# Performance work log

Measured on AMD Instinct MI355X. Metric: run time of the kernel, lower is better.

Reference implementation:

```python
import jax, jax.numpy as jnp
import numpy as np

N, D, H1, K = 4096, 128, 256, 128


def setup_inputs() -> dict:
    key = jax.random.key(0)
    ks = jax.random.split(key, 8)
    A = jax.random.uniform(ks[3], (D, D), dtype=jnp.float32)
    A = A * (1.0 - jnp.eye(D, dtype=jnp.float32))  # DAG prob mask, no self-loops
    return {
        "x": jax.random.normal(ks[0], (N, D), dtype=jnp.float32),
        "weight": jax.random.normal(ks[1], (D, D), dtype=jnp.float32) * 0.1,
        "bias": jax.random.normal(ks[2], (1, D), dtype=jnp.float32) * 0.1,
        "A": A,
        "W1": jax.random.normal(ks[4], (D, H1), dtype=jnp.float32) * 0.1,
        "b1": jax.random.normal(ks[5], (H1,), dtype=jnp.float32) * 0.1,
        "W2": jax.random.normal(ks[6], (H1, K), dtype=jnp.float32) * 0.1,
        "b2": jax.random.normal(ks[7], (K,), dtype=jnp.float32) * 0.1,
    }


def reference(x, weight, bias, A, W1, b1, W2, b2):
    # to_adj (eval path): masked weights
    W = weight * A                                   # [D, D]
    y = x @ W + bias                                 # [N, D]
    # __expand__ builds diag(y[n]) [N,D,D]; since e[n,i,:] = y[n,i]*I[i,:],
    # the first Linear collapses to a per-row scaling of W1 (same math, fused):
    # e @ W1 -> y[n,i] * W1[i,:]
    h1 = jax.nn.relu(y[:, :, None] * W1[None, :, :] + b1)   # [N, D, H1]
    f = (h1 @ W2 + b2).sum(axis=2)                   # [N, D] (sum over output dim)
    # h_func, method='gnn'
    I = jnp.eye(D, dtype=x.dtype)
    A2 = jnp.square(W)
    M = I + A2 / D
    E = jnp.linalg.matrix_power(M, D - 1)
    h_val = (E.T * M).sum() - D
    # l1_reg (same prob mask in eval)
    reg = jnp.abs(W).sum()
    return (f, h_val, reg)
```

## Files before the change

kernel.cpp:

```cpp
#include <hip/hip_runtime.h>

#define NN 4096
#define DD 128
#define HH1 256

#define WS_S    0
#define WS_S2   16384
#define WS_S3   32768
#define WS_S4   49152
#define WS_W    65536
#define WS_B2S  82688
#define WS_TACC 82696
#define WS_DONE 82708
#define WS_REGP 82712
#define WS_XT   99328
#define WS_TH   623616
#define WS_A    656384
#define WS_B    689280
#define WS_YT   722176
#define WS_REQ_FLOATS 1246464
#define WS_REQ_BYTES  (WS_REQ_FLOATS * 4UL)

#define O_S    0
#define O_S2   16384
#define O_S3   32768
#define O_S4   49152
#define O_W2S  65536
#define O_B2S  65792
#define O_TACC 65808
#define O_DONE 65824
#define O_REGP 65840

__device__ __forceinline__ float waveReduce(float v) {
#pragma unroll
  for (int off = 32; off > 0; off >>= 1) v += __shfl_down(v, off, 64);
  return v;
}


__global__ __launch_bounds__(256) void kA4(
    const float* __restrict__ weight, const float* __restrict__ Amat,
    const float* __restrict__ b2, const float* __restrict__ x,
    float* __restrict__ ws) {
  const int b = blockIdx.x, tid = threadIdx.x;
  __shared__ float s_lds[DD * DD];
  if (b < 64) {
    const float4* w4 = (const float4*)weight;
    const float4* a4 = (const float4*)Amat;
    float4* s4 = (float4*)s_lds;
    const float inv = 1.0f / 128.0f;
    for (int e = tid; e < DD * DD / 4; e += 256) {
      float4 wv = w4[e], av = a4[e], o;
      float t;
      t = wv.x * av.x; o.x = t * t * inv;
      t = wv.y * av.y; o.y = t * t * inv;
      t = wv.z * av.z; o.z = t * t * inv;
      t = wv.w * av.w; o.w = t * t * inv;
      s4[e] = o;
    }
    __syncthreads();
    const int i = (b << 1) + (tid >> 7), j = tid & 127;
    const float* row = &s_lds[i * DD];
    float acc = 0.f;
#pragma unroll 8
    for (int k = 0; k < DD; ++k) acc = fmaf(row[k], s_lds[k * DD + j], acc);
    ws[WS_S2 + i * DD + j] = acc;
  } else if (b < 72) {
    const int base = (b - 64) * 2048;
    const float inv = 1.0f / 128.0f;
    for (int e = tid; e < 2048; e += 256) {
      const int idx = base + e;
      const float w = weight[idx] * Amat[idx];
      ws[WS_W + idx] = w;
      ws[WS_S + idx] = w * w * inv;
    }
  } else if (b == 72) {
    __shared__ float red[4];
    float v = (tid < 128) ? b2[tid] : 0.f;
    v = waveReduce(v);
    if ((tid & 63) == 0) red[tid >> 6] = v;
    __syncthreads();
    if (tid == 0) ws[WS_B2S] = (red[0] + red[1]) + (red[2] + red[3]);
    if (tid >= 64 && tid < 74) ws[WS_TACC + (tid - 64)] = 0.f;
    if (tid == 96) *(unsigned int*)(ws + WS_DONE) = 0u;
  } else if (b < 81) {
    const int bb = b - 73;
    const int base = bb * 2048;
    float s = 0.f;
    for (int e = tid; e < 2048; e += 256) {
      const int idx = base + e;
      s += fabsf(weight[idx] * Amat[idx]);
    }
    s = waveReduce(s);
    __shared__ float red2[4];
    if ((tid & 63) == 0) red2[tid >> 6] = s;
    __syncthreads();
    if (tid == 0) ws[WS_REGP + bb] = (red2[0] + red2[1]) + (red2[2] + red2[3]);
  } else {
    float* xs = s_lds;
    const int n0 = (b - 81) * 64;
    const float4* x4 = (const float4*)x;
    for (int e = tid; e < 2048; e += 256) {
      const int r = e >> 5, c = e & 31;
      const float4 v = x4[(n0 + r) * 32 + c];
      float* p = &xs[r * 133 + (c << 2)];
      p[0] = v.x; p[1] = v.y; p[2] = v.z; p[3] = v.w;
    }
    __syncthreads();
    float* xT = ws + WS_XT;
    const int c = tid & 15, ks = tid >> 4;
#pragma unroll
    for (int m = 0; m < 8; ++m) {
      const int k = ks + (m << 4);
      float4 o;
      o.x = xs[((c << 2) + 0) * 133 + k];
      o.y = xs[((c << 2) + 1) * 133 + k];
      o.z = xs[((c << 2) + 2) * 133 + k];
      o.w = xs[((c << 2) + 3) * 133 + k];
      *(float4*)&xT[k * NN + n0 + (c << 2)] = o;
    }
  }
}

__global__ __launch_bounds__(256) void kB5(const float* __restrict__ bias,
                                           const float* __restrict__ W1,
                                           const float* __restrict__ b1v,
                                           const float* __restrict__ W2,
                                           float* __restrict__ ws) {
  const int tid = threadIdx.x;
  if (blockIdx.x < 128) {
    const int sb = blockIdx.x;
    const bool isS4 = sb >= 64;
    const int mb = isS4 ? sb - 64 : sb;
    const float* __restrict__ L = ws + WS_S2;
    const float* __restrict__ R = ws + (isS4 ? WS_S2 : WS_S);
    float* __restrict__ O = ws + (isS4 ? WS_S4 : WS_S3);
    const int i = (mb << 1) + (tid >> 7), j = tid & 127;
    float acc = 0.f;
#pragma unroll 8
    for (int k = 0; k < DD; ++k) acc = fmaf(L[i * DD + k], R[k * DD + j], acc);
    O[i * DD + j] = acc;
    return;
  }
  if (blockIdx.x < 384) {
    const int kb = blockIdx.x - 128;
    const int n0 = (kb & 15) << 8, i0 = (kb >> 4) << 3;
    const int n = n0 + tid;
    const float* __restrict__ xT = ws + WS_XT;
    const float* __restrict__ Wm = ws + WS_W;
    float* __restrict__ yT = ws + WS_YT;
    float acc[8];
#pragma unroll
    for (int q = 0; q < 8; ++q) acc[q] = 0.f;
#pragma unroll 8
    for (int k = 0; k < DD; ++k) {
      const float xv = xT[k * NN + n];
      const float* Wk = Wm + k * DD + i0;
#pragma unroll
      for (int q = 0; q < 8; ++q) acc[q] = fmaf(Wk[q], xv, acc[q]);
    }
#pragma unroll
    for (int q = 0; q < 8; ++q) yT[(i0 + q) * NN + n] = acc[q] + bias[i0 + q];
    return;
  }
  const int i = blockIdx.x - 384;
  __shared__ float kT[256], kS[256], kC[256];
  __shared__ float redb[8];
  const int j = tid;
  const float4* r = (const float4*)(W2 + j * 128);
  float4 s4v = make_float4(0.f, 0.f, 0.f, 0.f);
#pragma unroll 8
  for (int k = 0; k < 32; ++k) {
    const float4 v = r[k];
    s4v.x += v.x; s4v.y += v.y; s4v.z += v.z; s4v.w += v.w;
  }
  const float w2s = (s4v.x + s4v.y) + (s4v.z + s4v.w);
  const float w = W1[i * HH1 + j];
  const float bj = b1v[j];
  const float s = w * w2s, c = bj * w2s;
  float th, ds, dc, bs, bc;
  if (w > 0.f) {
    th = -bj / w; ds = s; dc = c; bs = 0.f; bc = 0.f;
  } else if (w < 0.f) {
    th = -bj / w; ds = -s; dc = -c; bs = s; bc = c;
  } else {
    th = 3.4e38f; ds = 0.f; dc = 0.f; bs = 0.f; bc = fmaxf(bj, 0.f) * w2s;
  }
  {
    const float rs = waveReduce(bs), rc = waveReduce(bc);
    if ((tid & 63) == 0) {
      redb[tid >> 6] = rs;
      redb[4 + (tid >> 6)] = rc;
    }
  }
  kT[tid] = th; kS[tid] = ds; kC[tid] = dc;
  __syncthreads();
  const float b_s = (redb[0] + redb[1]) + (redb[2] + redb[3]);
  const float b_c = (redb[4] + redb[5]) + (redb[6] + redb[7]);
  int rank = 0;
  float accS = 0.f, accC = 0.f;
  for (int jj = 0; jj < 256; ++jj) {
    const float thj = kT[jj];
    const float dsj = kS[jj], dcj = kC[jj];
    const bool le = (thj < th) || (thj == th && jj <= j);
    if (le) {
      ++rank;
      accS += dsj;
      accC += dcj;
    }
  }
  ws[WS_TH + i * 256 + (rank - 1)] = th;
  ws[WS_A + i * 257 + rank] = b_s + accS;
  ws[WS_B + i * 257 + rank] = b_c + accC;
  if (tid == 0) {
    ws[WS_A + i * 257] = b_s;
    ws[WS_B + i * 257] = b_c;
  }
}

__global__ __launch_bounds__(256) void kC7(float* __restrict__ ws,
                                           float* __restrict__ out) {
  const int tid = threadIdx.x;
  if (blockIdx.x < 512) {
    __shared__ float lT[4 * 256];
    __shared__ float lA[4 * 257];
    __shared__ float lB[4 * 257];
    __shared__ float ts[256 * 5];
    const int fb = blockIdx.x;
    const int n0 = (fb >> 5) << 8, i0 = (fb & 31) << 2;
    const int w = tid >> 6, l = tid & 63;
    const int iu = __builtin_amdgcn_readfirstlane(i0 + w);

#pragma unroll
    for (int q = 0; q < 4; ++q) {
      lT[(q << 8) + tid] = ws[WS_TH + (i0 + q) * 256 + tid];
      lA[q * 257 + tid] = ws[WS_A + (i0 + q) * 257 + tid];
      lB[q * 257 + tid] = ws[WS_B + (i0 + q) * 257 + tid];
      if (tid == 0) {
        lA[q * 257 + 256] = ws[WS_A + (i0 + q) * 257 + 256];
        lB[q * 257 + 256] = ws[WS_B + (i0 + q) * 257 + 256];
      }
    }
    const float* __restrict__ yT = ws + WS_YT;
    const float4 yv = *(const float4*)&yT[iu * NN + n0 + (l << 2)];
    const float sb2 = ws[WS_B2S];
    __syncthreads();

    const float* Tw = &lT[w << 8];
    const float* Aw = &lA[w * 257];
    const float* Bw = &lB[w * 257];
    const float yq4[4] = {yv.x, yv.y, yv.z, yv.w};
#pragma unroll
    for (int q = 0; q < 4; ++q) {
      const float yq = yq4[q];
      int m = 0;
#pragma unroll
      for (int st = 128; st > 0; st >>= 1) {
        if (Tw[m + st - 1] <= yq) m += st;
      }
      const float f = fmaf(Aw[m], yq, Bw[m]) + sb2;
      ts[((l << 2) + q) * 5 + w] = f;
    }
    __syncthreads();
    const int m = tid;
    float4 o;
    o.x = ts[m * 5 + 0]; o.y = ts[m * 5 + 1];
    o.z = ts[m * 5 + 2]; o.w = ts[m * 5 + 3];
    *(float4*)&out[(n0 + m) * DD + i0] = o;
    return;
  }
  const int tb = blockIdx.x - 512;
  const int i = (tb << 1) + (tid >> 7), j = tid & 127;
  const float* S1 = ws + WS_S;
  const float* S2 = ws + WS_S2;
  const float* S3 = ws + WS_S3;
  const float* S4 = ws + WS_S4;
  const float a1 = S1[i * DD + j], a2 = S2[i * DD + j], a3 = S3[i * DD + j];
  const float b1t = S1[j * DD + i], b2t = S2[j * DD + i],
              b3t = S3[j * DD + i], b4t = S4[j * DD + i];
  float e7 = 0.f;
#pragma unroll 8
  for (int k = 0; k < DD; ++k) e7 = fmaf(S3[i * DD + k], S4[k * DD + j], e7);
  float c[10];
  c[0] = a1 * b1t; c[1] = a2 * b1t; c[2] = a2 * b2t; c[3] = a3 * b2t;
  c[4] = a3 * b3t; c[5] = a3 * b4t; c[6] = e7 * b1t; c[7] = e7 * b2t;
  c[8] = e7 * b3t; c[9] = e7 * b4t;
  __shared__ float red[4][10];
#pragma unroll
  for (int m = 0; m < 10; ++m) {
    const float v = waveReduce(c[m]);
    if ((tid & 63) == 0) red[tid >> 6][m] = v;
  }
  __syncthreads();
  if (tid == 0) {
    float* tacc = ws + WS_TACC;
    for (int m = 0; m < 10; ++m)
      atomicAdd(&tacc[m], (red[0][m] + red[1][m]) + (red[2][m] + red[3][m]));
    __threadfence();
    unsigned int* done = (unsigned int*)(ws + WS_DONE);
    const unsigned int old = atomicAdd(done, 1u);
    if (old == 63u) {
      __threadfence();
      double h = 0.0, C = 8128.0;
      for (int kk = 2; kk <= 11; ++kk) {
        const float tv = atomicAdd(&tacc[kk - 2], 0.0f);
        h += C * (double)tv;
        C = C * (double)(128 - kk) / (double)(kk + 1);
      }
      float reg = 0.f;
      for (int m = 0; m < 8; ++m) reg += ws[WS_REGP + m];
      out[NN * DD] = (float)h;
      out[NN * DD + 1] = reg;
    }
  }
}

__global__ __launch_bounds__(256) void kA_old(
    const float* __restrict__ weight, const float* __restrict__ Amat,
    const float* __restrict__ W2, const float* __restrict__ b2,
    float* __restrict__ ws) {
  const int b = blockIdx.x, tid = threadIdx.x;
  if (b < 64) {
    __shared__ float s_lds[DD * DD];
    const float4* w4 = (const float4*)weight;
    const float4* a4 = (const float4*)Amat;
    float4* s4 = (float4*)s_lds;
    const float inv = 1.0f / 128.0f;
    for (int e = tid; e < DD * DD / 4; e += 256) {
      float4 wv = w4[e], av = a4[e], o;
      float t;
      t = wv.x * av.x; o.x = t * t * inv;
      t = wv.y * av.y; o.y = t * t * inv;
      t = wv.z * av.z; o.z = t * t * inv;
      t = wv.w * av.w; o.w = t * t * inv;
      s4[e] = o;
    }
    __syncthreads();
    const int i = (b << 1) + (tid >> 7), j = tid & 127;
    const float* row = &s_lds[i * DD];
    float acc = 0.f;
#pragma unroll 8
    for (int k = 0; k < DD; ++k) acc = fmaf(row[k], s_lds[k * DD + j], acc);
    ws[O_S2 + i * DD + j] = acc;
  } else if (b < 72) {
    const int base = (b - 64) * 2048;
    const float inv = 1.0f / 128.0f;
    for (int e = tid; e < 2048; e += 256) {
      const int idx = base + e;
      const float w = weight[idx] * Amat[idx];
      ws[O_S + idx] = w * w * inv;
    }
  } else if (b == 72) {
    const float4* r = (const float4*)(W2 + tid * 128);
    float4 s4 = make_float4(0.f, 0.f, 0.f, 0.f);
#pragma unroll 8
    for (int k = 0; k < 32; ++k) {
      const float4 v = r[k];
      s4.x += v.x; s4.y += v.y; s4.z += v.z; s4.w += v.w;
    }
    ws[O_W2S + tid] = (s4.x + s4.y) + (s4.z + s4.w);
  } else if (b == 73) {
    __shared__ float red[4];
    float v = (tid < 128) ? b2[tid] : 0.f;
    v = waveReduce(v);
    if ((tid & 63) == 0) red[tid >> 6] = v;
    __syncthreads();
    if (tid == 0) ws[O_B2S] = (red[0] + red[1]) + (red[2] + red[3]);
    if (tid >= 64 && tid < 74) ws[O_TACC + (tid - 64)] = 0.f;
    if (tid == 96) *(unsigned int*)(ws + O_DONE) = 0u;
  } else {
    const int bb = b - 74;
    const int base = bb * 2048;
    float s = 0.f;
    for (int e = tid; e < 2048; e += 256) {
      const int idx = base + e;
      s += fabsf(weight[idx] * Amat[idx]);
    }
    s = waveReduce(s);
    __shared__ float red[4];
    if ((tid & 63) == 0) red[tid >> 6] = s;
    __syncthreads();
    if (tid == 0) ws[O_REGP + bb] = (red[0] + red[1]) + (red[2] + red[3]);
  }
}

__global__ __launch_bounds__(256) void kB_old(
    const float* __restrict__ x, const float* __restrict__ weight,
    const float* __restrict__ Amat, const float* __restrict__ bias,
    const float* __restrict__ W1, const float* __restrict__ b1v,
    float* __restrict__ ws, float* __restrict__ out) {
  const int tid = threadIdx.x;
  if (blockIdx.x < 128) {
    const int sb = blockIdx.x;
    const bool isS4 = sb >= 64;
    const int mb = isS4 ? sb - 64 : sb;
    const float* __restrict__ L = ws + O_S2;
    const float* __restrict__ R = ws + (isS4 ? O_S2 : O_S);
    float* __restrict__ O = ws + (isS4 ? O_S4 : O_S3);
    const int i = (mb << 1) + (tid >> 7), j = tid & 127;
    float acc = 0.f;
#pragma unroll 8
    for (int k = 0; k < DD; ++k) acc = fmaf(L[i * DD + k], R[k * DD + j], acc);
    O[i * DD + j] = acc;
    return;
  }
  __shared__ float xs[64 * 132];
  __shared__ float4 fq[4 * 256];
  __shared__ float wcol[4 * 128];
  __shared__ float ts[64 * 5];
  const int fb = blockIdx.x - 128;
  const int i0 = (fb & 31) << 2, n0 = (fb >> 5) << 6;
  const float4* x4 = (const float4*)x;
  for (int e = tid; e < 64 * 32; e += 256) {
    const int r = e >> 5, c = e & 31;
    *(float4*)&xs[r * 132 + (c << 2)] = x4[(n0 + r) * 32 + c];
  }
  for (int e = tid; e < 512; e += 256) {
    const int w = e >> 7, k = e & 127;
    const int gi = k * DD + i0 + w;
    wcol[(w << 7) + k] = weight[gi] * Amat[gi];
  }
  const float* w2s = ws + O_W2S;
  for (int e = tid; e < 1024; e += 256) {
    const int w = e >> 8, j = e & 255;
    fq[(w << 8) + j] = make_float4(W1[(i0 + w) * HH1 + j], b1v[j], w2s[j], 0.f);
  }
  __syncthreads();
  const int w = tid >> 6, l = tid & 63;
  float t = bias[i0 + w];
  const float4* xr = (const float4*)&xs[l * 132];
  const float4* wc = (const float4*)&wcol[w << 7];
#pragma unroll
  for (int k = 0; k < 32; ++k) {
    const float4 xv = xr[k], wv = wc[k];
    t = fmaf(xv.x, wv.x, t);
    t = fmaf(xv.y, wv.y, t);
    t = fmaf(xv.z, wv.z, t);
    t = fmaf(xv.w, wv.w, t);
  }
  float acc = ws[O_B2S];
  const float4* fp = &fq[w << 8];
#pragma unroll 8
  for (int j = 0; j < HH1; ++j) {
    const float4 c = fp[j];
    acc = fmaf(fmaxf(fmaf(t, c.x, c.y), 0.f), c.z, acc);
  }
  ts[l * 5 + w] = acc;
  __syncthreads();
  if (tid < 64) {
    const float4 o = make_float4(ts[tid * 5 + 0], ts[tid * 5 + 1],
                                 ts[tid * 5 + 2], ts[tid * 5 + 3]);
    *(float4*)&out[(n0 + tid) * DD + i0] = o;
  }
}

__global__ __launch_bounds__(256) void kC_old(float* __restrict__ ws,
                                              float* __restrict__ out) {
  const int tid = threadIdx.x;
  const int i = (blockIdx.x << 1) + (tid >> 7), j = tid & 127;
  const float* S1 = ws + O_S;
  const float* S2 = ws + O_S2;
  const float* S3 = ws + O_S3;
  const float* S4 = ws + O_S4;
  const float a1 = S1[i * DD + j], a2 = S2[i * DD + j], a3 = S3[i * DD + j];
  const float b1t = S1[j * DD + i], b2t = S2[j * DD + i],
              b3t = S3[j * DD + i], b4t = S4[j * DD + i];
  float e7 = 0.f;
#pragma unroll 8
  for (int k = 0; k < DD; ++k) e7 = fmaf(S3[i * DD + k], S4[k * DD + j], e7);
  float c[10];
  c[0] = a1 * b1t; c[1] = a2 * b1t; c[2] = a2 * b2t; c[3] = a3 * b2t;
  c[4] = a3 * b3t; c[5] = a3 * b4t; c[6] = e7 * b1t; c[7] = e7 * b2t;
  c[8] = e7 * b3t; c[9] = e7 * b4t;
  __shared__ float red[4][10];
#pragma unroll
  for (int m = 0; m < 10; ++m) {
    const float v = waveReduce(c[m]);
    if ((tid & 63) == 0) red[tid >> 6][m] = v;
  }
  __syncthreads();
  if (tid == 0) {
    float* tacc = ws + O_TACC;
    for (int m = 0; m < 10; ++m)
      atomicAdd(&tacc[m], (red[0][m] + red[1][m]) + (red[2][m] + red[3][m]));
    __threadfence();
    unsigned int* done = (unsigned int*)(ws + O_DONE);
    const unsigned int old = atomicAdd(done, 1u);
    if (old == 63u) {
      __threadfence();
      double h = 0.0, C = 8128.0;
      for (int kk = 2; kk <= 11; ++kk) {
        const float tv = atomicAdd(&tacc[kk - 2], 0.0f);
        h += C * (double)tv;
        C = C * (double)(128 - kk) / (double)(kk + 1);
      }
      float reg = 0.f;
      for (int m = 0; m < 8; ++m) reg += ws[O_REGP + m];
      out[NN * DD] = (float)h;
      out[NN * DD + 1] = reg;
    }
  }
}

extern "C" void kernel_launch(void* const* d_in, const int* in_sizes, int n_in,
                              void* d_out, int out_size, void* d_ws,
                              size_t ws_size, hipStream_t stream) {
  const float* x      = (const float*)d_in[0];
  const float* weight = (const float*)d_in[1];
  const float* bias   = (const float*)d_in[2];
  const float* Amat   = (const float*)d_in[3];
  const float* W1     = (const float*)d_in[4];
  const float* b1v    = (const float*)d_in[5];
  const float* W2     = (const float*)d_in[6];
  const float* b2     = (const float*)d_in[7];
  float* out = (float*)d_out;
  float* ws  = (float*)d_ws;

  if (ws_size >= WS_REQ_BYTES) {
    kA4<<<145, 256, 0, stream>>>(weight, Amat, b2, x, ws);
    kB5<<<512, 256, 0, stream>>>(bias, W1, b1v, W2, ws);
    kC7<<<576, 256, 0, stream>>>(ws, out);
  } else {
    kA_old<<<82, 256, 0, stream>>>(weight, Amat, W2, b2, ws);
    kB_old<<<128 + 2048, 256, 0, stream>>>(x, weight, Amat, bias, W1, b1v, ws,
                                           out);
    kC_old<<<64, 256, 0, stream>>>(ws, out);
  }
}
```

Measured before the change: 120.2 us.

## Move y=xW GEMM and threshold sort into first kernel, drop x transpose

The x@W projection and the per-i threshold/prefix-sum blocks move from the second kernel into the first. The GEMM now stages x tiles transposed in LDS and computes weight*A on the fly, so the global x transpose (xT) and the masked-W buffer are no longer written or read back. The second kernel now only computes the S3/S4 matrix products. This trims global memory traffic and makes the launches more even, at the cost of a larger first grid and some redundant weight*A multiplies per block.

```diff
diff --git a/kernel.cpp b/kernel.cpp
--- a/kernel.cpp
+++ b/kernel.cpp
@@ -8,12 +8,10 @@
 #define WS_S2   16384
 #define WS_S3   32768
 #define WS_S4   49152
-#define WS_W    65536
 #define WS_B2S  82688
 #define WS_TACC 82696
 #define WS_DONE 82708
 #define WS_REGP 82712
-#define WS_XT   99328
 #define WS_TH   623616
 #define WS_A    656384
 #define WS_B    689280
@@ -38,16 +36,18 @@
 }
 
 
-__global__ __launch_bounds__(256) void kA4(
+__global__ __launch_bounds__(256) void kA5(
     const float* __restrict__ weight, const float* __restrict__ Amat,
     const float* __restrict__ b2, const float* __restrict__ x,
+    const float* __restrict__ bias, const float* __restrict__ W1,
+    const float* __restrict__ b1v, const float* __restrict__ W2,
     float* __restrict__ ws) {
   const int b = blockIdx.x, tid = threadIdx.x;
-  __shared__ float s_lds[DD * DD];
+  __shared__ float smem[DD * DD];
   if (b < 64) {
     const float4* w4 = (const float4*)weight;
     const float4* a4 = (const float4*)Amat;
-    float4* s4 = (float4*)s_lds;
+    float4* s4 = (float4*)smem;
     const float inv = 1.0f / 128.0f;
     for (int e = tid; e < DD * DD / 4; e += 256) {
       float4 wv = w4[e], av = a4[e], o;
@@ -60,10 +60,10 @@
     }
     __syncthreads();
     const int i = (b << 1) + (tid >> 7), j = tid & 127;
-    const float* row = &s_lds[i * DD];
+    const float* row = &smem[i * DD];
     float acc = 0.f;
 #pragma unroll 8
-    for (int k = 0; k < DD; ++k) acc = fmaf(row[k], s_lds[k * DD + j], acc);
+    for (int k = 0; k < DD; ++k) acc = fmaf(row[k], smem[k * DD + j], acc);
     ws[WS_S2 + i * DD + j] = acc;
   } else if (b < 72) {
     const int base = (b - 64) * 2048;
@@ -71,11 +71,10 @@
     for (int e = tid; e < 2048; e += 256) {
       const int idx = base + e;
       const float w = weight[idx] * Amat[idx];
-      ws[WS_W + idx] = w;
       ws[WS_S + idx] = w * w * inv;
     }
   } else if (b == 72) {
-    __shared__ float red[4];
+    float* red = smem;
     float v = (tid < 128) ? b2[tid] : 0.f;
     v = waveReduce(v);
     if ((tid & 63) == 0) red[tid >> 6] = v;
@@ -92,130 +91,119 @@
       s += fabsf(weight[idx] * Amat[idx]);
     }
     s = waveReduce(s);
-    __shared__ float red2[4];
+    float* red2 = smem;
     if ((tid & 63) == 0) red2[tid >> 6] = s;
     __syncthreads();
     if (tid == 0) ws[WS_REGP + bb] = (red2[0] + red2[1]) + (red2[2] + red2[3]);
+  } else if (b < 209) {
+    const int i = b - 81;
+    float* kT = smem;
+    float* kS = smem + 256;
+    float* kC = smem + 512;
+    float* redb = smem + 768;
+    const int j = tid;
+    const float4* r = (const float4*)(W2 + j * 128);
+    float4 s4v = make_float4(0.f, 0.f, 0.f, 0.f);
+#pragma unroll 8
+    for (int k = 0; k < 32; ++k) {
+      const float4 v = r[k];
+      s4v.x += v.x; s4v.y += v.y; s4v.z += v.z; s4v.w += v.w;
+    }
+    const float w2s = (s4v.x + s4v.y) + (s4v.z + s4v.w);
+    const float w = W1[i * HH1 + j];
+    const float bj = b1v[j];
+    const float s = w * w2s, c = bj * w2s;
+    float th, ds, dc, bs, bc;
+    if (w > 0.f) {
+      th = -bj / w; ds = s; dc = c; bs = 0.f; bc = 0.f;
+    } else if (w < 0.f) {
+      th = -bj / w; ds = -s; dc = -c; bs = s; bc = c;
+    } else {
+      th = 3.4e38f; ds = 0.f; dc = 0.f; bs = 0.f; bc = fmaxf(bj, 0.f) * w2s;
+    }
+    {
+      const float rs = waveReduce(bs), rc = waveReduce(bc);
+      if ((tid & 63) == 0) {
+        redb[tid >> 6] = rs;
+        redb[4 + (tid >> 6)] = rc;
+      }
+    }
+    kT[tid] = th; kS[tid] = ds; kC[tid] = dc;
+    __syncthreads();
+    const float b_s = (redb[0] + redb[1]) + (redb[2] + redb[3]);
+    const float b_c = (redb[4] + redb[5]) + (redb[6] + redb[7]);
+    int rank = 0;
+    float accS = 0.f, accC = 0.f;
+    for (int jj = 0; jj < 256; ++jj) {
+      const float thj = kT[jj];
+      const float dsj = kS[jj], dcj = kC[jj];
+      const bool le = (thj < th) || (thj == th && jj <= j);
+      if (le) {
+        ++rank;
+        accS += dsj;
+        accC += dcj;
+      }
+    }
+    ws[WS_TH + i * 256 + (rank - 1)] = th;
+    ws[WS_A + i * 257 + rank] = b_s + accS;
+    ws[WS_B + i * 257 + rank] = b_c + accC;
+    if (tid == 0) {
+      ws[WS_A + i * 257] = b_s;
+      ws[WS_B + i * 257] = b_c;
+    }
   } else {
-    float* xs = s_lds;
-    const int n0 = (b - 81) * 64;
+    const int kb = b - 209;
+    const int n0 = (kb & 15) << 8, i0 = (kb >> 4) << 3;
+    float* xs = smem;
     const float4* x4 = (const float4*)x;
-    for (int e = tid; e < 2048; e += 256) {
-      const int r = e >> 5, c = e & 31;
-      const float4 v = x4[(n0 + r) * 32 + c];
-      float* p = &xs[r * 133 + (c << 2)];
-      p[0] = v.x; p[1] = v.y; p[2] = v.z; p[3] = v.w;
-    }
-    __syncthreads();
-    float* xT = ws + WS_XT;
-    const int c = tid & 15, ks = tid >> 4;
-#pragma unroll
-    for (int m = 0; m < 8; ++m) {
-      const int k = ks + (m << 4);
-      float4 o;
-      o.x = xs[((c << 2) + 0) * 133 + k];
-      o.y = xs[((c << 2) + 1) * 133 + k];
-      o.z = xs[((c << 2) + 2) * 133 + k];
-      o.w = xs[((c << 2) + 3) * 133 + k];
-      *(float4*)&xT[k * NN + n0 + (c << 2)] = o;
-    }
-  }
-}
-
-__global__ __launch_bounds__(256) void kB5(const float* __restrict__ bias,
-                                           const float* __restrict__ W1,
-                                           const float* __restrict__ b1v,
-                                           const float* __restrict__ W2,
-                                           float* __restrict__ ws) {
+    float acc[8];
+#pragma unroll
+    for (int q = 0; q < 8; ++q) acc[q] = 0.f;
+    for (int kc = 0; kc < 4; ++kc) {
+      __syncthreads();
+#pragma unroll
+      for (int m = 0; m < 8; ++m) {
+        const int e = tid + (m << 8);
+        const int r = e >> 3, c = e & 7;
+        const float4 v = x4[(n0 + r) * 32 + (kc << 3) + c];
+        const int k4 = c << 2;
+        xs[(k4 + 0) * 257 + r] = v.x;
+        xs[(k4 + 1) * 257 + r] = v.y;
+        xs[(k4 + 2) * 257 + r] = v.z;
+        xs[(k4 + 3) * 257 + r] = v.w;
+      }
+      __syncthreads();
+#pragma unroll
+      for (int kk = 0; kk < 32; ++kk) {
+        const int k = (kc << 5) + kk;
+        const float xv = xs[kk * 257 + tid];
+        const float* wr = weight + k * DD + i0;
+        const float* ar = Amat + k * DD + i0;
+#pragma unroll
+        for (int q = 0; q < 8; ++q)
+          acc[q] = fmaf(wr[q] * ar[q], xv, acc[q]);
+      }
+    }
+    float* yT = ws + WS_YT;
+#pragma unroll
+    for (int q = 0; q < 8; ++q)
+      yT[(i0 + q) * NN + n0 + tid] = acc[q] + bias[i0 + q];
+  }
+}
+
+__global__ __launch_bounds__(256) void kS34(float* __restrict__ ws) {
   const int tid = threadIdx.x;
-  if (blockIdx.x < 128) {
-    const int sb = blockIdx.x;
-    const bool isS4 = sb >= 64;
-    const int mb = isS4 ? sb - 64 : sb;
-    const float* __restrict__ L = ws + WS_S2;
-    const float* __restrict__ R = ws + (isS4 ? WS_S2 : WS_S);
-    float* __restrict__ O = ws + (isS4 ? WS_S4 : WS_S3);
-    const int i = (mb << 1) + (tid >> 7), j = tid & 127;
-    float acc = 0.f;
-#pragma unroll 8
-    for (int k = 0; k < DD; ++k) acc = fmaf(L[i * DD + k], R[k * DD + j], acc);
-    O[i * DD + j] = acc;
-    return;
-  }
-  if (blockIdx.x < 384) {
-    const int kb = blockIdx.x - 128;
-    const int n0 = (kb & 15) << 8, i0 = (kb >> 4) << 3;
-    const int n = n0 + tid;
-    const float* __restrict__ xT = ws + WS_XT;
-    const float* __restrict__ Wm = ws + WS_W;
-    float* __restrict__ yT = ws + WS_YT;
-    float acc[8];
-#pragma unroll
-    for (int q = 0; q < 8; ++q) acc[q] = 0.f;
-#pragma unroll 8
-    for (int k = 0; k < DD; ++k) {
-      const float xv = xT[k * NN + n];
-      const float* Wk = Wm + k * DD + i0;
-#pragma unroll
-      for (int q = 0; q < 8; ++q) acc[q] = fmaf(Wk[q], xv, acc[q]);
-    }
-#pragma unroll
-    for (int q = 0; q < 8; ++q) yT[(i0 + q) * NN + n] = acc[q] + bias[i0 + q];
-    return;
-  }
-  const int i = blockIdx.x - 384;
-  __shared__ float kT[256], kS[256], kC[256];
-  __shared__ float redb[8];
-  const int j = tid;
-  const float4* r = (const float4*)(W2 + j * 128);
-  float4 s4v = make_float4(0.f, 0.f, 0.f, 0.f);
-#pragma unroll 8
-  for (int k = 0; k < 32; ++k) {
-    const float4 v = r[k];
-    s4v.x += v.x; s4v.y += v.y; s4v.z += v.z; s4v.w += v.w;
-  }
-  const float w2s = (s4v.x + s4v.y) + (s4v.z + s4v.w);
-  const float w = W1[i * HH1 + j];
-  const float bj = b1v[j];
-  const float s = w * w2s, c = bj * w2s;
-  float th, ds, dc, bs, bc;
-  if (w > 0.f) {
-    th = -bj / w; ds = s; dc = c; bs = 0.f; bc = 0.f;
-  } else if (w < 0.f) {
-    th = -bj / w; ds = -s; dc = -c; bs = s; bc = c;
-  } else {
-    th = 3.4e38f; ds = 0.f; dc = 0.f; bs = 0.f; bc = fmaxf(bj, 0.f) * w2s;
-  }
-  {
-    const float rs = waveReduce(bs), rc = waveReduce(bc);
-    if ((tid & 63) == 0) {
-      redb[tid >> 6] = rs;
-      redb[4 + (tid >> 6)] = rc;
-    }
-  }
-  kT[tid] = th; kS[tid] = ds; kC[tid] = dc;
-  __syncthreads();
-  const float b_s = (redb[0] + redb[1]) + (redb[2] + redb[3]);
-  const float b_c = (redb[4] + redb[5]) + (redb[6] + redb[7]);
-  int rank = 0;
-  float accS = 0.f, accC = 0.f;
-  for (int jj = 0; jj < 256; ++jj) {
-    const float thj = kT[jj];
-    const float dsj = kS[jj], dcj = kC[jj];
-    const bool le = (thj < th) || (thj == th && jj <= j);
-    if (le) {
-      ++rank;
-      accS += dsj;
-      accC += dcj;
-    }
-  }
-  ws[WS_TH + i * 256 + (rank - 1)] = th;
-  ws[WS_A + i * 257 + rank] = b_s + accS;
-  ws[WS_B + i * 257 + rank] = b_c + accC;
-  if (tid == 0) {
-    ws[WS_A + i * 257] = b_s;
-    ws[WS_B + i * 257] = b_c;
-  }
+  const int sb = blockIdx.x;
+  const bool isS4 = sb >= 64;
+  const int mb = isS4 ? sb - 64 : sb;
+  const float* __restrict__ L = ws + WS_S2;
+  const float* __restrict__ R = ws + (isS4 ? WS_S2 : WS_S);
+  float* __restrict__ O = ws + (isS4 ? WS_S4 : WS_S3);
+  const int i = (mb << 1) + (tid >> 7), j = tid & 127;
+  float acc = 0.f;
+#pragma unroll 8
+  for (int k = 0; k < DD; ++k) acc = fmaf(L[i * DD + k], R[k * DD + j], acc);
+  O[i * DD + j] = acc;
 }
 
 __global__ __launch_bounds__(256) void kC7(float* __restrict__ ws,
@@ -517,8 +505,8 @@
   float* ws  = (float*)d_ws;
 
   if (ws_size >= WS_REQ_BYTES) {
-    kA4<<<145, 256, 0, stream>>>(weight, Amat, b2, x, ws);
-    kB5<<<512, 256, 0, stream>>>(bias, W1, b1v, W2, ws);
+    kA5<<<465, 256, 0, stream>>>(weight, Amat, b2, x, bias, W1, b1v, W2, ws);
+    kS34<<<128, 256, 0, stream>>>(ws);
     kC7<<<576, 256, 0, stream>>>(ws, out);
   } else {
     kA_old<<<82, 256, 0, stream>>>(weight, Amat, W2, b2, ws);
```

Measured after the change: 133.4 us. 1.11x slower.
